# Optimization experiments

Measured on AMD Instinct MI355X. Metric: run time of the kernel, lower is better.

## Reference

```python
import jax, jax.numpy as jnp
import numpy as np

B, F, N, J, L_LAYERS = 16, 16, 1024, 8, 3


def setup_inputs() -> dict:
    key = jax.random.key(0)
    k1, k2, k3 = jax.random.split(key, 3)
    x = jax.random.normal(k1, (B, F, N), dtype=jnp.float32)
    psi = jax.random.normal(k2, (J, N, N), dtype=jnp.float32) / np.sqrt(N)
    lowpass = jax.random.uniform(k3, (N,), dtype=jnp.float32) / N
    return {"x": x, "psi": psi, "lowpass": lowpass, "L": L_LAYERS}


def reference(x, psi, lowpass, L):
    # x: [B, F, N] graph signals; psi: [J, N, N] wavelet filterbank; lowpass: [N]
    Bs, Fs, Ns = x.shape
    # layer-0 lowpass projection: phi = x @ lowpass -> [B, F, 1]
    phi = jnp.einsum('bfn,n->bf', x, lowpass)[:, :, None]
    S_x = x[:, None, :, :]  # [B, K=1, F, N]
    for _ in range(1, L):
        # apply all J wavelets to all K branches, then abs nonlinearity
        # (branch order k-major, j-minor matches the torch cat loop)
        S_x = jnp.abs(jnp.einsum('bkfn,jnm->bkjfm', S_x, psi))
        K = S_x.shape[1] * S_x.shape[2]
        S_x = S_x.reshape(Bs, K, Fs, Ns)
        # lowpass-pool every branch: [B, F, K]
        phi_l = jnp.einsum('bkfn,n->bfk', S_x, lowpass)
        phi = jnp.concatenate([phi, phi_l], axis=2)
    return phi  # [B, F, 1 + J + J^2 + ... + J^(L-1)]
```

## Files before the change

### kernel.cpp

```cpp
#include <hip/hip_runtime.h>

#define ND 1024
#define NNE (ND*ND)

typedef float f32x4 __attribute__((ext_vector_type(4)));
typedef int i32x4 __attribute__((ext_vector_type(4)));
typedef int i32x8 __attribute__((ext_vector_type(8)));

__device__ __forceinline__ void gload_lds16(const void* g, void* l) {
  __builtin_amdgcn_global_load_lds(
      (const __attribute__((address_space(1))) void*)g,
      (__attribute__((address_space(3))) void*)l, 16, 0, 0);
}

__global__ __launch_bounds__(256)
void prep_kernel(const float* __restrict__ psi, unsigned char* __restrict__ out8,
                 const float* __restrict__ x, const float* __restrict__ lp,
                 unsigned char* __restrict__ x8, float* __restrict__ phi) {
  __shared__ __align__(16) unsigned char T[128 * 144];
  __shared__ float ws[4];
  const int blk = blockIdx.x;
  const int tid = threadIdx.x;

  if (blk >= 512) {
    int row = blk - 512;
    if (tid >= 1 && tid < 73) phi[row * 73 + tid] = 0.f;
    float4 v = reinterpret_cast<const float4*>(x + (size_t)row * ND)[tid];
    float4 l = reinterpret_cast<const float4*>(lp)[tid];
    int pk = __builtin_amdgcn_cvt_pk_fp8_f32(v.x, v.y, 0, false);
    pk = __builtin_amdgcn_cvt_pk_fp8_f32(v.z, v.w, pk, true);
    reinterpret_cast<unsigned int*>(x8 + (size_t)row * ND)[tid] = (unsigned int)pk;
    float s = v.x * l.x + v.y * l.y + v.z * l.z + v.w * l.w;
    #pragma unroll
    for (int off = 32; off; off >>= 1) s += __shfl_xor(s, off);
    if ((tid & 63) == 0) ws[tid >> 6] = s;
    __syncthreads();
    if (tid == 0) phi[row * 73] = ws[0] + ws[1] + ws[2] + ws[3];
    return;
  }

  const int j  = blk >> 6;
  const int t6 = blk & 63;
  const int tn = t6 >> 3, tm = t6 & 7;
  const int n0 = tn * 128, m0 = tm * 128;
  const float* src = psi + ((size_t)j << 20) + (size_t)n0 * ND + m0;

  const int rgrp = tid >> 5;
  const int c4   = (tid & 31) << 2;
  #pragma unroll
  for (int it = 0; it < 16; ++it) {
    int nl = it * 8 + rgrp;
    float4 v = *reinterpret_cast<const float4*>(src + (size_t)nl * ND + c4);
    int p01 = __builtin_amdgcn_cvt_pk_fp8_f32(v.x, v.y, 0, false);
    int p23 = __builtin_amdgcn_cvt_pk_fp8_f32(v.z, v.w, 0, false);
    T[(c4 + 0) * 144 + nl] = (unsigned char)(p01 & 0xff);
    T[(c4 + 1) * 144 + nl] = (unsigned char)((p01 >> 8) & 0xff);
    T[(c4 + 2) * 144 + nl] = (unsigned char)(p23 & 0xff);
    T[(c4 + 3) * 144 + nl] = (unsigned char)((p23 >> 8) & 0xff);
  }
  __syncthreads();

  unsigned char* dst = out8 + ((size_t)j << 20) + (size_t)m0 * ND + n0;
  const int mrow = tid >> 3;
  const int ch   = (tid & 7) << 4;
  #pragma unroll
  for (int it = 0; it < 4; ++it) {
    int ml = it * 32 + mrow;
    uint4 v = *reinterpret_cast<const uint4*>(&T[ml * 144 + ch]);
    *reinterpret_cast<uint4*>(dst + (size_t)ml * ND + ch) = v;
  }
}

__device__ __forceinline__ i32x8 dsr_frag8(const unsigned char* base, int r, int l4) {
  int s0 = l4 * 2;
  i32x4 lo = *reinterpret_cast<const i32x4*>(base + r * 128 + ((s0 ^ (r & 7)) << 4));
  i32x4 hi = *reinterpret_cast<const i32x4*>(base + r * 128 + (((s0 + 1) ^ (r & 7)) << 4));
  return __builtin_shufflevector(lo, hi, 0, 1, 2, 3, 4, 5, 6, 7);
}

__device__ __forceinline__ void stage128(const unsigned char* __restrict__ A, int row0,
                                         const unsigned char* __restrict__ Bj, int n0,
                                         int k0, unsigned char* As, unsigned char* Bs,
                                         int tid) {
  #pragma unroll
  for (int p = 0; p < 4; ++p) {
    int c = p * 256 + tid;
    int r = c >> 3;
    int s = (c & 7) ^ (r & 7);
    gload_lds16(A + (size_t)(row0 + r) * ND + k0 + (s << 4), As + c * 16);
  }
  #pragma unroll
  for (int p = 0; p < 4; ++p) {
    int c = p * 256 + tid;
    int r = c >> 3;
    int s = (c & 7) ^ (r & 7);
    gload_lds16(Bj + (size_t)(n0 + r) * ND + k0 + (s << 4), Bs + c * 16);
  }
}

__device__ __forceinline__ void compute128(const unsigned char* As, const unsigned char* Bs,
                                           f32x4 (&acc)[4][4],
                                           int wrow, int wcol, int l15, int l4) {
  i32x8 a[4], b[4];
  #pragma unroll
  for (int m = 0; m < 4; ++m)
    a[m] = dsr_frag8(As, wrow * 64 + m * 16 + l15, l4);
  #pragma unroll
  for (int n = 0; n < 4; ++n)
    b[n] = dsr_frag8(Bs, wcol * 64 + n * 16 + l15, l4);
  #pragma unroll
  for (int m = 0; m < 4; ++m)
    #pragma unroll
    for (int n = 0; n < 4; ++n)
      acc[m][n] = __builtin_amdgcn_mfma_scale_f32_16x16x128_f8f6f4(
          a[m], b[n], acc[m][n], 0, 0, 0, 0x7f7f7f7f, 0, 0x7f7f7f7f);
}

__global__ __launch_bounds__(256, 2)
void gemm8_l1(const unsigned char* __restrict__ A,
              const unsigned char* __restrict__ BT,
              const float* __restrict__ lowpass,
              unsigned char* __restrict__ Sout,
              float* __restrict__ phi) {
  __shared__ __align__(16) unsigned char As0[128 * 128];
  __shared__ __align__(16) unsigned char As1[128 * 128];
  __shared__ __align__(16) unsigned char Bs0[128 * 128];
  __shared__ __align__(16) unsigned char Bs1[128 * 128];

  const int tid  = threadIdx.x;
  const int lane = tid & 63;
  const int w    = tid >> 6;
  const int wrow = w >> 1, wcol = w & 1;
  const int l15  = lane & 15, l4 = lane >> 4;

  const int wg = blockIdx.x;
  const int j  = wg & 7;
  const int t  = wg >> 3;
  const int mtile = t & 1, ntile = t >> 1;
  const int row0 = mtile * 128, n0 = ntile * 128;
  const unsigned char* Bj = BT + (size_t)j * NNE;

  f32x4 acc[4][4] = {};

  stage128(A, row0, Bj, n0, 0, As0, Bs0, tid);
  __syncthreads();

  #pragma unroll 1
  for (int k0 = 0; k0 < ND; k0 += 128) {
    const int cur = (k0 >> 7) & 1;
    const unsigned char* Ac = cur ? As1 : As0;
    const unsigned char* Bc = cur ? Bs1 : Bs0;
    if (k0 + 128 < ND)
      stage128(A, row0, Bj, n0, k0 + 128, cur ? As0 : As1, cur ? Bs0 : Bs1, tid);
    compute128(Ac, Bc, acc, wrow, wcol, l15, l4);
    __syncthreads();
  }

  float lp[4];
  #pragma unroll
  for (int n = 0; n < 4; ++n)
    lp[n] = lowpass[n0 + wcol * 64 + n * 16 + l15];

  #pragma unroll
  for (int m = 0; m < 4; ++m) {
    #pragma unroll
    for (int r = 0; r < 4; ++r) {
      int rg = row0 + wrow * 64 + m * 16 + l4 * 4 + r;
      float psum = 0.f;
      #pragma unroll
      for (int n = 0; n < 4; ++n) {
        float v = fabsf(acc[m][n][r]);
        psum += v * lp[n];
        int colg = n0 + wcol * 64 + n * 16 + l15;
        size_t si = ((size_t)((rg >> 4) * 8 + j) * 16 + (rg & 15)) * ND + colg;
        int pk = __builtin_amdgcn_cvt_pk_fp8_f32(v, v, 0, false);
        Sout[si] = (unsigned char)(pk & 0xff);
      }
      psum += __shfl_xor(psum, 1);
      psum += __shfl_xor(psum, 2);
      psum += __shfl_xor(psum, 4);
      psum += __shfl_xor(psum, 8);
      if (l15 == 0) {
        int pidx = rg * 73 + 1 + j;
        atomicAdd(&phi[pidx], psum);
      }
    }
  }
}


__device__ __forceinline__ void stage256(const unsigned char* __restrict__ A, int row0,
                                         const unsigned char* __restrict__ Bj, int n0,
                                         int k0, unsigned char* As, unsigned char* Bs,
                                         int tid) {
  #pragma unroll
  for (int p = 0; p < 4; ++p) {
    int c = p * 512 + tid;
    int r = c >> 3;
    int s = (c & 7) ^ (r & 7);
    gload_lds16(A + (size_t)(row0 + r) * ND + k0 + (s << 4), As + c * 16);
  }
  #pragma unroll
  for (int p = 0; p < 4; ++p) {
    int c = p * 512 + tid;
    int r = c >> 3;
    int s = (c & 7) ^ (r & 7);
    gload_lds16(Bj + (size_t)(n0 + r) * ND + k0 + (s << 4), Bs + c * 16);
  }
}

__device__ __forceinline__ void compute256(const unsigned char* As, const unsigned char* Bs,
                                           f32x4 (&acc)[8][4],
                                           int wrow, int wcol, int l15, int l4) {
  i32x8 b[4];
  #pragma unroll
  for (int n = 0; n < 4; ++n)
    b[n] = dsr_frag8(Bs, wcol * 64 + n * 16 + l15, l4);
  #pragma unroll
  for (int m = 0; m < 8; ++m) {
    i32x8 a = dsr_frag8(As, wrow * 128 + m * 16 + l15, l4);
    #pragma unroll
    for (int n = 0; n < 4; ++n)
      acc[m][n] = __builtin_amdgcn_mfma_scale_f32_16x16x128_f8f6f4(
          a, b[n], acc[m][n], 0, 0, 0, 0x7f7f7f7f, 0, 0x7f7f7f7f);
  }
}

__global__ __launch_bounds__(512, 1)
void gemm8_l2(const unsigned char* __restrict__ A,
              const unsigned char* __restrict__ BT,
              const float* __restrict__ lowpass,
              float* __restrict__ phi) {
  __shared__ __align__(16) unsigned char As0[256 * 128];
  __shared__ __align__(16) unsigned char As1[256 * 128];
  __shared__ __align__(16) unsigned char Bs0[256 * 128];
  __shared__ __align__(16) unsigned char Bs1[256 * 128];

  const int tid  = threadIdx.x;
  const int lane = tid & 63;
  const int w    = tid >> 6;
  const int wrow = w >> 2, wcol = w & 3;
  const int l15  = lane & 15, l4 = lane >> 4;

  const int wg = blockIdx.x;
  const int j  = wg & 7;
  const int t  = wg >> 3;
  const int mtile = t & 7, ntile = t >> 3;
  const int row0 = mtile * 256, n0 = ntile * 256;
  const unsigned char* Bj = BT + (size_t)j * NNE;

  f32x4 acc[8][4] = {};

  stage256(A, row0, Bj, n0, 0, As0, Bs0, tid);
  __syncthreads();

  #pragma unroll 1
  for (int k0 = 0; k0 < ND; k0 += 128) {
    const int cur = (k0 >> 7) & 1;
    const unsigned char* Ac = cur ? As1 : As0;
    const unsigned char* Bc = cur ? Bs1 : Bs0;
    if (k0 + 128 < ND)
      stage256(A, row0, Bj, n0, k0 + 128, cur ? As0 : As1, cur ? Bs0 : Bs1, tid);
    compute256(Ac, Bc, acc, wrow, wcol, l15, l4);
    __syncthreads();
  }

  float lp[4];
  #pragma unroll
  for (int n = 0; n < 4; ++n)
    lp[n] = lowpass[n0 + wcol * 64 + n * 16 + l15];

  #pragma unroll
  for (int m = 0; m < 8; ++m) {
    #pragma unroll
    for (int r = 0; r < 4; ++r) {
      int rg = row0 + wrow * 128 + m * 16 + l4 * 4 + r;
      float psum = 0.f;
      #pragma unroll
      for (int n = 0; n < 4; ++n)
        psum += fabsf(acc[m][n][r]) * lp[n];
      psum += __shfl_xor(psum, 1);
      psum += __shfl_xor(psum, 2);
      psum += __shfl_xor(psum, 4);
      psum += __shfl_xor(psum, 8);
      if (l15 == 0) {
        int pidx = ((rg >> 7) * 16 + (rg & 15)) * 73 + 9 + ((rg >> 4) & 7) * 8 + j;
        atomicAdd(&phi[pidx], psum);
      }
    }
  }
}

extern "C" void kernel_launch(void* const* d_in, const int* in_sizes, int n_in,
                              void* d_out, int out_size, void* d_ws, size_t ws_size,
                              hipStream_t stream) {
  (void)in_sizes; (void)n_in; (void)ws_size; (void)out_size;
  const float* x       = (const float*)d_in[0];
  const float* psi     = (const float*)d_in[1];
  const float* lowpass = (const float*)d_in[2];
  float* phi = (float*)d_out;

  unsigned char* x8    = (unsigned char*)d_ws;
  unsigned char* psiT8 = (unsigned char*)((char*)d_ws + (1u << 20));
  unsigned char* S1f8  = (unsigned char*)((char*)d_ws + (10u << 20));

  prep_kernel<<<768, 256, 0, stream>>>(psi, psiT8, x, lowpass, x8, phi);

  gemm8_l1<<<128, 256, 0, stream>>>(x8, psiT8, lowpass, S1f8, phi);

  gemm8_l2<<<256, 512, 0, stream>>>(S1f8, psiT8, lowpass, phi);
}
```

Measured before the change: 60.20 us.

## Fuse prep and both GEMM layers into one cooperative persistent kernel

Merges the psi transpose/fp8 conversion, the layer-1 GEMM and the layer-2 GEMM into a single cooperative kernel of 256 workgroups, separated by grid-wide syncs. This removes two kernel launch gaps and tail effects between stages. The prep transpose now goes through a padded 32-bit LDS tile, and layer 1 uses 512-thread blocks with smaller per-wave tiles. In exchange, the kernel pays grid-sync costs and leaves half the workgroups idle during layer 1.

```diff
diff --git a/kernel.cpp b/kernel.cpp
--- a/kernel.cpp
+++ b/kernel.cpp
@@ -1,4 +1,7 @@
 #include <hip/hip_runtime.h>
+#include <hip/hip_cooperative_groups.h>
+
+namespace cg = cooperative_groups;
 
 #define ND 1024
 #define NNE (ND*ND)
@@ -11,64 +14,6 @@
   __builtin_amdgcn_global_load_lds(
       (const __attribute__((address_space(1))) void*)g,
       (__attribute__((address_space(3))) void*)l, 16, 0, 0);
-}
-
-__global__ __launch_bounds__(256)
-void prep_kernel(const float* __restrict__ psi, unsigned char* __restrict__ out8,
-                 const float* __restrict__ x, const float* __restrict__ lp,
-                 unsigned char* __restrict__ x8, float* __restrict__ phi) {
-  __shared__ __align__(16) unsigned char T[128 * 144];
-  __shared__ float ws[4];
-  const int blk = blockIdx.x;
-  const int tid = threadIdx.x;
-
-  if (blk >= 512) {
-    int row = blk - 512;
-    if (tid >= 1 && tid < 73) phi[row * 73 + tid] = 0.f;
-    float4 v = reinterpret_cast<const float4*>(x + (size_t)row * ND)[tid];
-    float4 l = reinterpret_cast<const float4*>(lp)[tid];
-    int pk = __builtin_amdgcn_cvt_pk_fp8_f32(v.x, v.y, 0, false);
-    pk = __builtin_amdgcn_cvt_pk_fp8_f32(v.z, v.w, pk, true);
-    reinterpret_cast<unsigned int*>(x8 + (size_t)row * ND)[tid] = (unsigned int)pk;
-    float s = v.x * l.x + v.y * l.y + v.z * l.z + v.w * l.w;
-    #pragma unroll
-    for (int off = 32; off; off >>= 1) s += __shfl_xor(s, off);
-    if ((tid & 63) == 0) ws[tid >> 6] = s;
-    __syncthreads();
-    if (tid == 0) phi[row * 73] = ws[0] + ws[1] + ws[2] + ws[3];
-    return;
-  }
-
-  const int j  = blk >> 6;
-  const int t6 = blk & 63;
-  const int tn = t6 >> 3, tm = t6 & 7;
-  const int n0 = tn * 128, m0 = tm * 128;
-  const float* src = psi + ((size_t)j << 20) + (size_t)n0 * ND + m0;
-
-  const int rgrp = tid >> 5;
-  const int c4   = (tid & 31) << 2;
-  #pragma unroll
-  for (int it = 0; it < 16; ++it) {
-    int nl = it * 8 + rgrp;
-    float4 v = *reinterpret_cast<const float4*>(src + (size_t)nl * ND + c4);
-    int p01 = __builtin_amdgcn_cvt_pk_fp8_f32(v.x, v.y, 0, false);
-    int p23 = __builtin_amdgcn_cvt_pk_fp8_f32(v.z, v.w, 0, false);
-    T[(c4 + 0) * 144 + nl] = (unsigned char)(p01 & 0xff);
-    T[(c4 + 1) * 144 + nl] = (unsigned char)((p01 >> 8) & 0xff);
-    T[(c4 + 2) * 144 + nl] = (unsigned char)(p23 & 0xff);
-    T[(c4 + 3) * 144 + nl] = (unsigned char)((p23 >> 8) & 0xff);
-  }
-  __syncthreads();
-
-  unsigned char* dst = out8 + ((size_t)j << 20) + (size_t)m0 * ND + n0;
-  const int mrow = tid >> 3;
-  const int ch   = (tid & 7) << 4;
-  #pragma unroll
-  for (int it = 0; it < 4; ++it) {
-    int ml = it * 32 + mrow;
-    uint4 v = *reinterpret_cast<const uint4*>(&T[ml * 144 + ch]);
-    *reinterpret_cast<uint4*>(dst + (size_t)ml * ND + ch) = v;
-  }
 }
 
 __device__ __forceinline__ i32x8 dsr_frag8(const unsigned char* base, int r, int l4) {
@@ -78,214 +23,234 @@
   return __builtin_shufflevector(lo, hi, 0, 1, 2, 3, 4, 5, 6, 7);
 }
 
-__device__ __forceinline__ void stage128(const unsigned char* __restrict__ A, int row0,
-                                         const unsigned char* __restrict__ Bj, int n0,
-                                         int k0, unsigned char* As, unsigned char* Bs,
-                                         int tid) {
-  #pragma unroll
-  for (int p = 0; p < 4; ++p) {
-    int c = p * 256 + tid;
-    int r = c >> 3;
-    int s = (c & 7) ^ (r & 7);
-    gload_lds16(A + (size_t)(row0 + r) * ND + k0 + (s << 4), As + c * 16);
-  }
-  #pragma unroll
-  for (int p = 0; p < 4; ++p) {
-    int c = p * 256 + tid;
-    int r = c >> 3;
-    int s = (c & 7) ^ (r & 7);
-    gload_lds16(Bj + (size_t)(n0 + r) * ND + k0 + (s << 4), Bs + c * 16);
-  }
-}
-
-__device__ __forceinline__ void compute128(const unsigned char* As, const unsigned char* Bs,
-                                           f32x4 (&acc)[4][4],
-                                           int wrow, int wcol, int l15, int l4) {
-  i32x8 a[4], b[4];
-  #pragma unroll
-  for (int m = 0; m < 4; ++m)
-    a[m] = dsr_frag8(As, wrow * 64 + m * 16 + l15, l4);
-  #pragma unroll
-  for (int n = 0; n < 4; ++n)
-    b[n] = dsr_frag8(Bs, wcol * 64 + n * 16 + l15, l4);
-  #pragma unroll
-  for (int m = 0; m < 4; ++m)
-    #pragma unroll
-    for (int n = 0; n < 4; ++n)
-      acc[m][n] = __builtin_amdgcn_mfma_scale_f32_16x16x128_f8f6f4(
-          a[m], b[n], acc[m][n], 0, 0, 0, 0x7f7f7f7f, 0, 0x7f7f7f7f);
-}
-
-__global__ __launch_bounds__(256, 2)
-void gemm8_l1(const unsigned char* __restrict__ A,
-              const unsigned char* __restrict__ BT,
-              const float* __restrict__ lowpass,
-              unsigned char* __restrict__ Sout,
-              float* __restrict__ phi) {
-  __shared__ __align__(16) unsigned char As0[128 * 128];
-  __shared__ __align__(16) unsigned char As1[128 * 128];
-  __shared__ __align__(16) unsigned char Bs0[128 * 128];
-  __shared__ __align__(16) unsigned char Bs1[128 * 128];
-
+__global__ __launch_bounds__(512, 1)
+void mega_kernel(const float* __restrict__ psi, const float* __restrict__ x,
+                 const float* __restrict__ lowpass,
+                 unsigned char* __restrict__ psiT8, unsigned char* __restrict__ x8,
+                 unsigned char* __restrict__ S1f8, float* __restrict__ phi) {
+  __shared__ __align__(16) unsigned char SMEM[131072];
+  unsigned char* As0 = SMEM;
+  unsigned char* As1 = SMEM + 32768;
+  unsigned char* Bs0 = SMEM + 65536;
+  unsigned char* Bs1 = SMEM + 98304;
+  unsigned*      Tu  = (unsigned*)SMEM;
+  float*         ws  = (float*)(SMEM + 65536);
+
+  const int wg   = blockIdx.x;
   const int tid  = threadIdx.x;
   const int lane = tid & 63;
   const int w    = tid >> 6;
-  const int wrow = w >> 1, wcol = w & 1;
   const int l15  = lane & 15, l4 = lane >> 4;
 
-  const int wg = blockIdx.x;
-  const int j  = wg & 7;
-  const int t  = wg >> 3;
-  const int mtile = t & 1, ntile = t >> 1;
-  const int row0 = mtile * 128, n0 = ntile * 128;
-  const unsigned char* Bj = BT + (size_t)j * NNE;
-
-  f32x4 acc[4][4] = {};
-
-  stage128(A, row0, Bj, n0, 0, As0, Bs0, tid);
+  if (tid >= 1 && tid < 73) phi[wg * 73 + tid] = 0.f;
+  if (tid < 256) {
+    float4 v = reinterpret_cast<const float4*>(x + (size_t)wg * ND)[tid];
+    float4 l = reinterpret_cast<const float4*>(lowpass)[tid];
+    int pk = __builtin_amdgcn_cvt_pk_fp8_f32(v.x, v.y, 0, false);
+    pk = __builtin_amdgcn_cvt_pk_fp8_f32(v.z, v.w, pk, true);
+    reinterpret_cast<unsigned*>(x8 + (size_t)wg * ND)[tid] = (unsigned)pk;
+    float s = v.x * l.x + v.y * l.y + v.z * l.z + v.w * l.w;
+    #pragma unroll
+    for (int off = 32; off; off >>= 1) s += __shfl_xor(s, off);
+    if ((tid & 63) == 0) ws[tid >> 6] = s;
+  }
   __syncthreads();
+  if (tid == 0) phi[wg * 73] = ws[0] + ws[1] + ws[2] + ws[3];
 
   #pragma unroll 1
-  for (int k0 = 0; k0 < ND; k0 += 128) {
-    const int cur = (k0 >> 7) & 1;
-    const unsigned char* Ac = cur ? As1 : As0;
-    const unsigned char* Bc = cur ? Bs1 : Bs0;
-    if (k0 + 128 < ND)
-      stage128(A, row0, Bj, n0, k0 + 128, cur ? As0 : As1, cur ? Bs0 : Bs1, tid);
-    compute128(Ac, Bc, acc, wrow, wcol, l15, l4);
-    __syncthreads();
-  }
-
-  float lp[4];
-  #pragma unroll
-  for (int n = 0; n < 4; ++n)
-    lp[n] = lowpass[n0 + wcol * 64 + n * 16 + l15];
-
-  #pragma unroll
-  for (int m = 0; m < 4; ++m) {
-    #pragma unroll
-    for (int r = 0; r < 4; ++r) {
-      int rg = row0 + wrow * 64 + m * 16 + l4 * 4 + r;
-      float psum = 0.f;
-      #pragma unroll
-      for (int n = 0; n < 4; ++n) {
-        float v = fabsf(acc[m][n][r]);
-        psum += v * lp[n];
-        int colg = n0 + wcol * 64 + n * 16 + l15;
-        size_t si = ((size_t)((rg >> 4) * 8 + j) * 16 + (rg & 15)) * ND + colg;
-        int pk = __builtin_amdgcn_cvt_pk_fp8_f32(v, v, 0, false);
-        Sout[si] = (unsigned char)(pk & 0xff);
-      }
-      psum += __shfl_xor(psum, 1);
-      psum += __shfl_xor(psum, 2);
-      psum += __shfl_xor(psum, 4);
-      psum += __shfl_xor(psum, 8);
-      if (l15 == 0) {
-        int pidx = rg * 73 + 1 + j;
-        atomicAdd(&phi[pidx], psum);
-      }
-    }
-  }
-}
-
-
-__device__ __forceinline__ void stage256(const unsigned char* __restrict__ A, int row0,
-                                         const unsigned char* __restrict__ Bj, int n0,
-                                         int k0, unsigned char* As, unsigned char* Bs,
-                                         int tid) {
-  #pragma unroll
-  for (int p = 0; p < 4; ++p) {
-    int c = p * 512 + tid;
-    int r = c >> 3;
-    int s = (c & 7) ^ (r & 7);
-    gload_lds16(A + (size_t)(row0 + r) * ND + k0 + (s << 4), As + c * 16);
-  }
-  #pragma unroll
-  for (int p = 0; p < 4; ++p) {
-    int c = p * 512 + tid;
-    int r = c >> 3;
-    int s = (c & 7) ^ (r & 7);
-    gload_lds16(Bj + (size_t)(n0 + r) * ND + k0 + (s << 4), Bs + c * 16);
-  }
-}
-
-__device__ __forceinline__ void compute256(const unsigned char* As, const unsigned char* Bs,
-                                           f32x4 (&acc)[8][4],
-                                           int wrow, int wcol, int l15, int l4) {
-  i32x8 b[4];
-  #pragma unroll
-  for (int n = 0; n < 4; ++n)
-    b[n] = dsr_frag8(Bs, wcol * 64 + n * 16 + l15, l4);
-  #pragma unroll
-  for (int m = 0; m < 8; ++m) {
-    i32x8 a = dsr_frag8(As, wrow * 128 + m * 16 + l15, l4);
+  for (int jj = 0; jj < 2; ++jj) {
+    const int t  = wg * 2 + jj;
+    const int j  = t >> 6;
+    const int t6 = t & 63;
+    const int tn = t6 >> 3, tm = t6 & 7;
+    const int n0 = tn * 128, m0 = tm * 128;
+    const float* src = psi + ((size_t)j << 20) + (size_t)n0 * ND + m0;
+    __syncthreads();
+    #pragma unroll
+    for (int it = 0; it < 8; ++it) {
+      int idx = it * 512 + tid;
+      int nl = idx >> 5, c4 = (idx & 31) << 2;
+      float4 v = *reinterpret_cast<const float4*>(src + (size_t)nl * ND + c4);
+      int pk = __builtin_amdgcn_cvt_pk_fp8_f32(v.x, v.y, 0, false);
+      pk = __builtin_amdgcn_cvt_pk_fp8_f32(v.z, v.w, pk, true);
+      Tu[nl * 33 + (c4 >> 2)] = (unsigned)pk;
+    }
+    __syncthreads();
+    unsigned char* dst = psiT8 + ((size_t)j << 20) + (size_t)m0 * ND + n0;
+    #pragma unroll
+    for (int it = 0; it < 8; ++it) {
+      int idx = it * 512 + tid;
+      int m = idx >> 5, nb = idx & 31;
+      int mq = m >> 2, mb = (m & 3) * 8;
+      unsigned b0 = (Tu[(4 * nb + 0) * 33 + mq] >> mb) & 0xffu;
+      unsigned b1 = (Tu[(4 * nb + 1) * 33 + mq] >> mb) & 0xffu;
+      unsigned b2 = (Tu[(4 * nb + 2) * 33 + mq] >> mb) & 0xffu;
+      unsigned b3 = (Tu[(4 * nb + 3) * 33 + mq] >> mb) & 0xffu;
+      *reinterpret_cast<unsigned*>(dst + (size_t)m * ND + 4 * nb) =
+          b0 | (b1 << 8) | (b2 << 16) | (b3 << 24);
+    }
+  }
+
+  cg::this_grid().sync();
+
+  if (wg < 128) {
+    const int j  = wg & 7;
+    const int t  = wg >> 3;
+    const int mtile = t & 1, ntile = t >> 1;
+    const int row0 = mtile * 128, n0 = ntile * 128;
+    const unsigned char* Bj = psiT8 + (size_t)j * NNE;
+    const int wrow = w >> 2, wcol = w & 3;
+
+    f32x4 acc[4][2] = {};
+
+    auto stage = [&](int k0, unsigned char* As, unsigned char* Bs) {
+      #pragma unroll
+      for (int p = 0; p < 2; ++p) {
+        int c = p * 512 + tid;
+        int r = c >> 3;
+        int s = (c & 7) ^ (r & 7);
+        gload_lds16(x8 + (size_t)(row0 + r) * ND + k0 + (s << 4), As + c * 16);
+      }
+      #pragma unroll
+      for (int p = 0; p < 2; ++p) {
+        int c = p * 512 + tid;
+        int r = c >> 3;
+        int s = (c & 7) ^ (r & 7);
+        gload_lds16(Bj + (size_t)(n0 + r) * ND + k0 + (s << 4), Bs + c * 16);
+      }
+    };
+
+    stage(0, As0, Bs0);
+    __syncthreads();
+
+    #pragma unroll 1
+    for (int k0 = 0; k0 < ND; k0 += 128) {
+      const int cur = (k0 >> 7) & 1;
+      const unsigned char* Ac = cur ? As1 : As0;
+      const unsigned char* Bc = cur ? Bs1 : Bs0;
+      if (k0 + 128 < ND) stage(k0 + 128, cur ? As0 : As1, cur ? Bs0 : Bs1);
+      i32x8 b[2];
+      #pragma unroll
+      for (int n = 0; n < 2; ++n)
+        b[n] = dsr_frag8(Bc, wcol * 32 + n * 16 + l15, l4);
+      #pragma unroll
+      for (int m = 0; m < 4; ++m) {
+        i32x8 a = dsr_frag8(Ac, wrow * 64 + m * 16 + l15, l4);
+        #pragma unroll
+        for (int n = 0; n < 2; ++n)
+          acc[m][n] = __builtin_amdgcn_mfma_scale_f32_16x16x128_f8f6f4(
+              a, b[n], acc[m][n], 0, 0, 0, 0x7f7f7f7f, 0, 0x7f7f7f7f);
+      }
+      __syncthreads();
+    }
+
+    float lp[2];
+    #pragma unroll
+    for (int n = 0; n < 2; ++n)
+      lp[n] = lowpass[n0 + wcol * 32 + n * 16 + l15];
+
+    #pragma unroll
+    for (int m = 0; m < 4; ++m) {
+      #pragma unroll
+      for (int r = 0; r < 4; ++r) {
+        int rg = row0 + wrow * 64 + m * 16 + l4 * 4 + r;
+        float psum = 0.f;
+        #pragma unroll
+        for (int n = 0; n < 2; ++n) {
+          float v = fabsf(acc[m][n][r]);
+          psum += v * lp[n];
+          int colg = n0 + wcol * 32 + n * 16 + l15;
+          size_t si = ((size_t)((rg >> 4) * 8 + j) * 16 + (rg & 15)) * ND + colg;
+          int pk = __builtin_amdgcn_cvt_pk_fp8_f32(v, v, 0, false);
+          S1f8[si] = (unsigned char)(pk & 0xff);
+        }
+        psum += __shfl_xor(psum, 1);
+        psum += __shfl_xor(psum, 2);
+        psum += __shfl_xor(psum, 4);
+        psum += __shfl_xor(psum, 8);
+        if (l15 == 0) {
+          atomicAdd(&phi[rg * 73 + 1 + j], psum);
+        }
+      }
+    }
+  }
+
+  cg::this_grid().sync();
+
+  {
+    const int j = wg & 7;
+    const int t = wg >> 3;
+    const int mtile = t & 7, ntile = t >> 3;
+    const int row0 = mtile * 256, n0 = ntile * 256;
+    const unsigned char* Bj = psiT8 + (size_t)j * NNE;
+    const int wrow = w >> 2, wcol = w & 3;
+
+    f32x4 acc[8][4] = {};
+
+    auto stage = [&](int k0, unsigned char* As, unsigned char* Bs) {
+      #pragma unroll
+      for (int p = 0; p < 4; ++p) {
+        int c = p * 512 + tid;
+        int r = c >> 3;
+        int s = (c & 7) ^ (r & 7);
+        gload_lds16(S1f8 + (size_t)(row0 + r) * ND + k0 + (s << 4), As + c * 16);
+      }
+      #pragma unroll
+      for (int p = 0; p < 4; ++p) {
+        int c = p * 512 + tid;
+        int r = c >> 3;
+        int s = (c & 7) ^ (r & 7);
+        gload_lds16(Bj + (size_t)(n0 + r) * ND + k0 + (s << 4), Bs + c * 16);
+      }
+    };
+
+    __syncthreads();
+    stage(0, As0, Bs0);
+    __syncthreads();
+
+    #pragma unroll 1
+    for (int k0 = 0; k0 < ND; k0 += 128) {
+      const int cur = (k0 >> 7) & 1;
+      const unsigned char* Ac = cur ? As1 : As0;
+      const unsigned char* Bc = cur ? Bs1 : Bs0;
+      if (k0 + 128 < ND) stage(k0 + 128, cur ? As0 : As1, cur ? Bs0 : Bs1);
+      i32x8 b[4];
+      #pragma unroll
+      for (int n = 0; n < 4; ++n)
+        b[n] = dsr_frag8(Bc, wcol * 64 + n * 16 + l15, l4);
+      #pragma unroll
+      for (int m = 0; m < 8; ++m) {
+        i32x8 a = dsr_frag8(Ac, wrow * 128 + m * 16 + l15, l4);
+        #pragma unroll
+        for (int n = 0; n < 4; ++n)
+          acc[m][n] = __builtin_amdgcn_mfma_scale_f32_16x16x128_f8f6f4(
+              a, b[n], acc[m][n], 0, 0, 0, 0x7f7f7f7f, 0, 0x7f7f7f7f);
+      }
+      __syncthreads();
+    }
+
+    float lp[4];
     #pragma unroll
     for (int n = 0; n < 4; ++n)
-      acc[m][n] = __builtin_amdgcn_mfma_scale_f32_16x16x128_f8f6f4(
-          a, b[n], acc[m][n], 0, 0, 0, 0x7f7f7f7f, 0, 0x7f7f7f7f);
-  }
-}
-
-__global__ __launch_bounds__(512, 1)
-void gemm8_l2(const unsigned char* __restrict__ A,
-              const unsigned char* __restrict__ BT,
-              const float* __restrict__ lowpass,
-              float* __restrict__ phi) {
-  __shared__ __align__(16) unsigned char As0[256 * 128];
-  __shared__ __align__(16) unsigned char As1[256 * 128];
-  __shared__ __align__(16) unsigned char Bs0[256 * 128];
-  __shared__ __align__(16) unsigned char Bs1[256 * 128];
-
-  const int tid  = threadIdx.x;
-  const int lane = tid & 63;
-  const int w    = tid >> 6;
-  const int wrow = w >> 2, wcol = w & 3;
-  const int l15  = lane & 15, l4 = lane >> 4;
-
-  const int wg = blockIdx.x;
-  const int j  = wg & 7;
-  const int t  = wg >> 3;
-  const int mtile = t & 7, ntile = t >> 3;
-  const int row0 = mtile * 256, n0 = ntile * 256;
-  const unsigned char* Bj = BT + (size_t)j * NNE;
-
-  f32x4 acc[8][4] = {};
-
-  stage256(A, row0, Bj, n0, 0, As0, Bs0, tid);
-  __syncthreads();
-
-  #pragma unroll 1
-  for (int k0 = 0; k0 < ND; k0 += 128) {
-    const int cur = (k0 >> 7) & 1;
-    const unsigned char* Ac = cur ? As1 : As0;
-    const unsigned char* Bc = cur ? Bs1 : Bs0;
-    if (k0 + 128 < ND)
-      stage256(A, row0, Bj, n0, k0 + 128, cur ? As0 : As1, cur ? Bs0 : Bs1, tid);
-    compute256(Ac, Bc, acc, wrow, wcol, l15, l4);
-    __syncthreads();
-  }
-
-  float lp[4];
-  #pragma unroll
-  for (int n = 0; n < 4; ++n)
-    lp[n] = lowpass[n0 + wcol * 64 + n * 16 + l15];
-
-  #pragma unroll
-  for (int m = 0; m < 8; ++m) {
-    #pragma unroll
-    for (int r = 0; r < 4; ++r) {
-      int rg = row0 + wrow * 128 + m * 16 + l4 * 4 + r;
-      float psum = 0.f;
-      #pragma unroll
-      for (int n = 0; n < 4; ++n)
-        psum += fabsf(acc[m][n][r]) * lp[n];
-      psum += __shfl_xor(psum, 1);
-      psum += __shfl_xor(psum, 2);
-      psum += __shfl_xor(psum, 4);
-      psum += __shfl_xor(psum, 8);
-      if (l15 == 0) {
-        int pidx = ((rg >> 7) * 16 + (rg & 15)) * 73 + 9 + ((rg >> 4) & 7) * 8 + j;
-        atomicAdd(&phi[pidx], psum);
+      lp[n] = lowpass[n0 + wcol * 64 + n * 16 + l15];
+
+    #pragma unroll
+    for (int m = 0; m < 8; ++m) {
+      #pragma unroll
+      for (int r = 0; r < 4; ++r) {
+        int rg = row0 + wrow * 128 + m * 16 + l4 * 4 + r;
+        float psum = 0.f;
+        #pragma unroll
+        for (int n = 0; n < 4; ++n)
+          psum += fabsf(acc[m][n][r]) * lp[n];
+        psum += __shfl_xor(psum, 1);
+        psum += __shfl_xor(psum, 2);
+        psum += __shfl_xor(psum, 4);
+        psum += __shfl_xor(psum, 8);
+        if (l15 == 0) {
+          int pidx = ((rg >> 7) * 16 + (rg & 15)) * 73 + 9 + ((rg >> 4) & 7) * 8 + j;
+          atomicAdd(&phi[pidx], psum);
+        }
       }
     }
   }
@@ -304,9 +269,7 @@
   unsigned char* psiT8 = (unsigned char*)((char*)d_ws + (1u << 20));
   unsigned char* S1f8  = (unsigned char*)((char*)d_ws + (10u << 20));
 
-  prep_kernel<<<768, 256, 0, stream>>>(psi, psiT8, x, lowpass, x8, phi);
-
-  gemm8_l1<<<128, 256, 0, stream>>>(x8, psiT8, lowpass, S1f8, phi);
-
-  gemm8_l2<<<256, 512, 0, stream>>>(S1f8, psiT8, lowpass, phi);
-}
+  void* args[] = { (void*)&psi, (void*)&x, (void*)&lowpass,
+                   (void*)&psiT8, (void*)&x8, (void*)&S1f8, (void*)&phi };
+  hipLaunchCooperativeKernel((void*)mega_kernel, dim3(256), dim3(512), args, 0, stream);
+}
```

Measured after the change: 135.5 us. +125.1%, slower.
